# Performance work log

Measured on AMD Instinct MI355X. Metric: run time of the kernel, lower is better.

## Reference

```python
import jax, jax.numpy as jnp
import numpy as np

CHANNELS = 128
M_MODES = 64
B = 128
N = 4096


def setup_inputs() -> dict:
    key = jax.random.key(0)
    k1, k2, k3 = jax.random.split(key, 3)
    h = jax.random.normal(k1, (B * N, CHANNELS), dtype=jnp.float32)
    U = jax.random.normal(k2, (B, N, M_MODES), dtype=jnp.float32)
    W = jax.random.normal(k3, (M_MODES, CHANNELS, CHANNELS), dtype=jnp.float32) * 0.02
    ptr = jnp.arange(B + 1, dtype=jnp.int64) * N  # equal-size segments
    return {"h": h, "U": U, "W": W, "ptr": ptr}


def reference(h, U, W, ptr):
    # U: [B, N, m]; h: [B*N, C]; W: [m, C, C]
    b, n, m = U.shape
    hb = h.reshape(b, n, -1)                              # [B, N, C]
    h_hat = jnp.einsum('bnm,bnc->bmc', U, hb)             # U^T h per graph
    out_hat = jnp.einsum('bmc,mco->bmo', h_hat, W)        # per-mode channel mix
    out = jnp.einsum('bnm,bmo->bno', U, out_hat)          # back to node space
    return out.reshape(h.shape)
```

## Files before the change

### kernel.cpp

```cpp
#include <hip/hip_runtime.h>

#define CH 128
#define MM 64
#define BB 128
#define NN 4096
#define KSPLIT 4
#define KCHUNK (NN / KSPLIT)
#define KSTEP 32
#define NSTEP (KCHUNK / KSTEP)

#define UBUF (KSTEP * MM)
#define HBUF (KSTEP * CH)
#define BUF  (UBUF + HBUF)
#define MMCH (MM * CH)

typedef __bf16 bf16x8 __attribute__((ext_vector_type(8)));
typedef float  f32x4  __attribute__((ext_vector_type(4)));

#define AS1(p) ((const __attribute__((address_space(1))) void*)(p))
#define AS3(p) ((__attribute__((address_space(3))) void*)(p))

__device__ __forceinline__ void gl_lds16(const float* g, float* l) {
    __builtin_amdgcn_global_load_lds(AS1(g), AS3(l), 16, 0, 0);
}

__global__ __launch_bounds__(256, 2) void k1_uth(const float* __restrict__ U,
                                                 const float* __restrict__ h,
                                                 float* __restrict__ hhp) {
    __shared__ float lds[2 * BUF];

    const int tid  = threadIdx.x;
    const int lane = tid & 63;
    const int wv   = tid >> 6;
    const int b    = blockIdx.x >> 2;
    const int ks   = blockIdx.x & 3;
    const int k0   = ks * KCHUNK;

    const int l15 = lane & 15;
    const int g   = lane >> 4;
    const int lk  = g * 8;

    const float* Ub = U + ((size_t)b * NN + k0) * MM;
    const float* hb = h + ((size_t)b * NN + k0) * CH;

    auto stage = [&](int s, int t) {
        float* dst = &lds[s * BUF];
        const float* us = Ub + (size_t)t * KSTEP * MM;
        const float* hs = hb + (size_t)t * KSTEP * CH;
        gl_lds16(us + tid * 4,        dst + tid * 4);
        gl_lds16(us + 1024 + tid * 4, dst + 1024 + tid * 4);
        gl_lds16(hs + tid * 4,        dst + UBUF + tid * 4);
        gl_lds16(hs + 1024 + tid * 4, dst + UBUF + 1024 + tid * 4);
        gl_lds16(hs + 2048 + tid * 4, dst + UBUF + 2048 + tid * 4);
        gl_lds16(hs + 3072 + tid * 4, dst + UBUF + 3072 + tid * 4);
    };

    f32x4 acc[4][2];
    #pragma unroll
    for (int t = 0; t < 4; ++t)
        #pragma unroll
        for (int ci = 0; ci < 2; ++ci)
            acc[t][ci] = (f32x4){0.f, 0.f, 0.f, 0.f};

    auto compute = [&](int s) {
        const float* P  = &lds[s * BUF];
        const float* Pa = P + lk * 64 + 2 * l15;
        const float* Pb = P + UBUF + lk * 128 + wv * 32 + 2 * l15;
        bf16x8 af[4], bfr[2];
        #pragma unroll
        for (int j = 0; j < 8; ++j) {
            float2 a0 = *(const float2*)(Pa + j * 64);
            float2 a1 = *(const float2*)(Pa + j * 64 + 32);
            float2 bv = *(const float2*)(Pb + j * 128);
            af[0][j]  = (__bf16)a0.x;
            af[1][j]  = (__bf16)a0.y;
            af[2][j]  = (__bf16)a1.x;
            af[3][j]  = (__bf16)a1.y;
            bfr[0][j] = (__bf16)bv.x;
            bfr[1][j] = (__bf16)bv.y;
        }
        #pragma unroll
        for (int t = 0; t < 4; ++t)
            #pragma unroll
            for (int ci = 0; ci < 2; ++ci)
                acc[t][ci] = __builtin_amdgcn_mfma_f32_16x16x32_bf16(
                    af[t], bfr[ci], acc[t][ci], 0, 0, 0);
    };

    stage(0, 0);
    #pragma unroll 1
    for (int t = 0; t < NSTEP; ++t) {
        if (t + 1 < NSTEP) {
            stage((t + 1) & 1, t + 1);
            asm volatile("s_waitcnt vmcnt(6)" ::: "memory");
        } else {
            asm volatile("s_waitcnt vmcnt(0)" ::: "memory");
        }
        __builtin_amdgcn_s_barrier();
        __builtin_amdgcn_sched_barrier(0);
        compute(t & 1);
        __builtin_amdgcn_s_barrier();
    }

    float* dst = hhp + (size_t)(b * KSPLIT + ks) * MMCH + wv * 32 + 2 * l15;
    #pragma unroll
    for (int t = 0; t < 4; ++t)
        #pragma unroll
        for (int r = 0; r < 4; ++r) {
            const int m = (t >> 1) * 32 + 2 * (g * 4 + r) + (t & 1);
            *(float2*)(dst + (size_t)m * CH) =
                make_float2(acc[t][0][r], acc[t][1][r]);
        }
}

__global__ __launch_bounds__(256) void k2_mix(const float* __restrict__ hhp,
                                              const float* __restrict__ W,
                                              __bf16* __restrict__ ohf) {
    __shared__ float hs[16][CH];
    const int tid  = threadIdx.x;
    const int o    = tid & 127;
    const int half = tid >> 7;
    const int m    = blockIdx.x;
    const int b0   = blockIdx.y * 16;

    #pragma unroll
    for (int i = 0; i < 8; ++i) {
        const int b = b0 + half * 8 + i;
        const float* src = hhp + ((size_t)(b * KSPLIT) * MM + m) * CH + o;
        float s = 0.f;
        #pragma unroll
        for (int ksi = 0; ksi < KSPLIT; ++ksi)
            s += src[(size_t)ksi * MMCH];
        hs[half * 8 + i][o] = s;
    }
    __syncthreads();

    float acc[8];
    #pragma unroll
    for (int i = 0; i < 8; ++i) acc[i] = 0.f;

    const float* Wm = W + (size_t)m * CH * CH;
    for (int c = 0; c < CH; ++c) {
        const float w = Wm[c * CH + o];
        #pragma unroll
        for (int i = 0; i < 8; ++i) acc[i] += hs[half * 8 + i][c] * w;
    }

    const int mt      = m >> 5;
    const int m5      = m & 31;
    const int lane_hi = m5 >> 3;
    const int j       = m5 & 7;
    const int ot      = o >> 4;
    const int lane    = lane_hi * 16 + (o & 15);
    const size_t eidx = ((size_t)(mt * 8 + ot) * 64 + lane) * 8 + j;

    #pragma unroll
    for (int i = 0; i < 8; ++i) {
        const int b = b0 + half * 8 + i;
        ohf[(size_t)b * 8192 + eidx] = (__bf16)acc[i];
    }
}

__global__ __launch_bounds__(256) void k3_back(const float* __restrict__ U,
                                               const __bf16* __restrict__ ohf,
                                               float* __restrict__ out) {
    const int tid  = threadIdx.x;
    const int lane = tid & 63;
    const int wv   = tid >> 6;
    const int n0   = blockIdx.x * 64;
    const int b    = blockIdx.y;

    const bf16x8* ohfb = (const bf16x8*)(ohf + (size_t)b * 8192);
    bf16x8 bf[2][8];
    #pragma unroll
    for (int mt = 0; mt < 2; ++mt)
        #pragma unroll
        for (int ot = 0; ot < 8; ++ot)
            bf[mt][ot] = ohfb[(mt * 8 + ot) * 64 + lane];

    const float* arow = U + ((size_t)b * NN + n0 + wv * 16 + (lane & 15)) * MM
                          + ((lane >> 4) << 3);
    bf16x8 af[2];
    #pragma unroll
    for (int mt = 0; mt < 2; ++mt) {
        float4 a0 = *(const float4*)(arow + mt * 32);
        float4 a1 = *(const float4*)(arow + mt * 32 + 4);
        af[mt][0] = (__bf16)a0.x; af[mt][1] = (__bf16)a0.y;
        af[mt][2] = (__bf16)a0.z; af[mt][3] = (__bf16)a0.w;
        af[mt][4] = (__bf16)a1.x; af[mt][5] = (__bf16)a1.y;
        af[mt][6] = (__bf16)a1.z; af[mt][7] = (__bf16)a1.w;
    }

    f32x4 acc[8];
    #pragma unroll
    for (int ot = 0; ot < 8; ++ot) acc[ot] = (f32x4){0.f, 0.f, 0.f, 0.f};

    #pragma unroll
    for (int ot = 0; ot < 8; ++ot) {
        acc[ot] = __builtin_amdgcn_mfma_f32_16x16x32_bf16(af[0], bf[0][ot], acc[ot], 0, 0, 0);
        acc[ot] = __builtin_amdgcn_mfma_f32_16x16x32_bf16(af[1], bf[1][ot], acc[ot], 0, 0, 0);
    }

    float* dst = out + ((size_t)b * NN + n0 + wv * 16 + (lane >> 4) * 4) * CH + (lane & 15);
    #pragma unroll
    for (int ot = 0; ot < 8; ++ot)
        #pragma unroll
        for (int r = 0; r < 4; ++r)
            dst[(size_t)r * CH + ot * 16] = acc[ot][r];
}

extern "C" void kernel_launch(void* const* d_in, const int* in_sizes, int n_in,
                              void* d_out, int out_size, void* d_ws, size_t ws_size,
                              hipStream_t stream) {
    const float* h = (const float*)d_in[0];
    const float* U = (const float*)d_in[1];
    const float* W = (const float*)d_in[2];
    float* out = (float*)d_out;

    float*  hhp = (float*)d_out;
    __bf16* ohf = (__bf16*)d_ws;

    k1_uth<<<BB * KSPLIT, 256, 0, stream>>>(U, h, hhp);
    k2_mix<<<dim3(MM, BB / 16), 256, 0, stream>>>(hhp, W, ohf);
    k3_back<<<dim3(NN / 64, BB), 256, 0, stream>>>(U, ohf, out);
}
```

Baseline: 210.6 us.

## Software-pipeline the three stages across batch chunks in a merged kernel

```diff
diff --git a/kernel.cpp b/kernel.cpp
--- a/kernel.cpp
+++ b/kernel.cpp
@@ -4,6 +4,8 @@
 #define MM 64
 #define BB 128
 #define NN 4096
+#define NC 4
+#define CB (BB / NC)
 #define KSPLIT 4
 #define KCHUNK (NN / KSPLIT)
 #define KSTEP 32
@@ -14,6 +16,10 @@
 #define BUF  (UBUF + HBUF)
 #define MMCH (MM * CH)
 
+#define N1C (CB * KSPLIT)
+#define N2C (64 * (CB / 16))
+#define N3C (64 * CB)
+
 typedef __bf16 bf16x8 __attribute__((ext_vector_type(8)));
 typedef float  f32x4  __attribute__((ext_vector_type(4)));
 
@@ -24,16 +30,14 @@
     __builtin_amdgcn_global_load_lds(AS1(g), AS3(l), 16, 0, 0);
 }
 
-__global__ __launch_bounds__(256, 2) void k1_uth(const float* __restrict__ U,
-                                                 const float* __restrict__ h,
-                                                 float* __restrict__ hhp) {
-    __shared__ float lds[2 * BUF];
-
+__device__ __forceinline__ void k1_body(float* lds, const float* __restrict__ U,
+                                        const float* __restrict__ h,
+                                        float* __restrict__ hhp, int bid, int c1) {
     const int tid  = threadIdx.x;
     const int lane = tid & 63;
     const int wv   = tid >> 6;
-    const int b    = blockIdx.x >> 2;
-    const int ks   = blockIdx.x & 3;
+    const int b    = c1 * CB + (bid >> 2);
+    const int ks   = bid & 3;
     const int k0   = ks * KCHUNK;
 
     const int l15 = lane & 15;
@@ -113,15 +117,15 @@
         }
 }
 
-__global__ __launch_bounds__(256) void k2_mix(const float* __restrict__ hhp,
-                                              const float* __restrict__ W,
-                                              __bf16* __restrict__ ohf) {
-    __shared__ float hs[16][CH];
+__device__ __forceinline__ void k2_body(float* lds, const float* __restrict__ hhp,
+                                        const float* __restrict__ W,
+                                        __bf16* __restrict__ ohf, int bid, int c2) {
+    float (*hs)[CH] = (float(*)[CH])lds;
     const int tid  = threadIdx.x;
     const int o    = tid & 127;
     const int half = tid >> 7;
-    const int m    = blockIdx.x;
-    const int b0   = blockIdx.y * 16;
+    const int m    = bid & 63;
+    const int b0   = c2 * CB + (bid >> 6) * 16;
 
     #pragma unroll
     for (int i = 0; i < 8; ++i) {
@@ -161,14 +165,14 @@
     }
 }
 
-__global__ __launch_bounds__(256) void k3_back(const float* __restrict__ U,
-                                               const __bf16* __restrict__ ohf,
-                                               float* __restrict__ out) {
+__device__ __forceinline__ void k3_body(const float* __restrict__ U,
+                                        const __bf16* __restrict__ ohf,
+                                        float* __restrict__ out, int bid, int c3) {
     const int tid  = threadIdx.x;
     const int lane = tid & 63;
     const int wv   = tid >> 6;
-    const int n0   = blockIdx.x * 64;
-    const int b    = blockIdx.y;
+    const int n0   = (bid & 63) * 64;
+    const int b    = c3 * CB + (bid >> 6);
 
     const bf16x8* ohfb = (const bf16x8*)(ohf + (size_t)b * 8192);
     bf16x8 bf[2][8];
@@ -209,6 +213,21 @@
             dst[(size_t)r * CH + ot * 16] = acc[ot][r];
 }
 
+__global__ __launch_bounds__(256, 2) void gsc_stage(
+    const float* __restrict__ U, const float* __restrict__ h,
+    const float* __restrict__ W, float* __restrict__ hhp,
+    __bf16* __restrict__ ohf, float* __restrict__ out,
+    int n1, int c1, int n2, int c2, int c3)
+{
+    __shared__ float lds[2 * BUF];
+    int bid = blockIdx.x;
+    if (bid < n1) { k1_body(lds, U, h, hhp, bid, c1); return; }
+    bid -= n1;
+    if (bid < n2) { k2_body(lds, hhp, W, ohf, bid, c2); return; }
+    bid -= n2;
+    k3_body(U, ohf, out, bid, c3);
+}
+
 extern "C" void kernel_launch(void* const* d_in, const int* in_sizes, int n_in,
                               void* d_out, int out_size, void* d_ws, size_t ws_size,
                               hipStream_t stream) {
@@ -217,10 +236,21 @@
     const float* W = (const float*)d_in[2];
     float* out = (float*)d_out;
 
-    float*  hhp = (float*)d_out;
+    float*  hhp = out + ((size_t)BB * NN * CH - (size_t)BB * KSPLIT * MMCH);
     __bf16* ohf = (__bf16*)d_ws;
 
-    k1_uth<<<BB * KSPLIT, 256, 0, stream>>>(U, h, hhp);
-    k2_mix<<<dim3(MM, BB / 16), 256, 0, stream>>>(hhp, W, ohf);
-    k3_back<<<dim3(NN / 64, BB), 256, 0, stream>>>(U, ohf, out);
-}
+    const int S[6][6] = {
+        {N1C, 0,   0, 0,   0, 0},
+        {N1C, 1, N2C, 0,   0, 0},
+        {N1C, 2, N2C, 1, N3C, 0},
+        {N1C, 3, N2C, 2, N3C, 1},
+        {  0, 0, N2C, 3, N3C, 2},
+        {  0, 0,   0, 0, N3C, 3},
+    };
+    for (int s = 0; s < 6; ++s) {
+        const int grid = S[s][0] + S[s][2] + S[s][4];
+        gsc_stage<<<grid, 256, 0, stream>>>(U, h, W, hhp, ohf, out,
+                                            S[s][0], S[s][1], S[s][2], S[s][3],
+                                            S[s][5]);
+    }
+}
```

Measured after the change: 194.4 us. 7.7% less time.
